# Kernel optimization log

Hardware: AMD Instinct MI355X
Metric: run time of the kernel (lower is better)

Reference implementation:

```python
import jax, jax.numpy as jnp
import numpy as np

B, S, D, H = 2, 2048, 1024, 16
HD = D // H          # 64
ROT = HD // 2        # 32

def _rope(x, cos, sin):
    # x: [B,S,H,HD] -> pairs [B,S,H,ROT,2]; cos/sin: [S,ROT] -> [1,S,1,ROT]
    x2 = x.reshape(x.shape[:3] + (ROT, 2))
    x0, x1 = x2[..., 0], x2[..., 1]
    c = cos[None, :, None, :]
    s = sin[None, :, None, :]
    out = jnp.stack([x0 * c - x1 * s, x1 * c + x0 * s], axis=-1)
    return out.reshape(x.shape)

def setup_inputs() -> dict:
    key = jax.random.key(0)
    ks = jax.random.split(key, 5)
    hidden_states = jax.random.normal(ks[0], (B, S, D), dtype=jnp.float32)
    # proper rotary cos/sin table: [S, ROT, 2]
    inv_freq = 1.0 / (10000.0 ** (np.arange(0, ROT, dtype=np.float32) / ROT))
    t = np.arange(S, dtype=np.float32)
    ang = np.outer(t, inv_freq)  # [S, ROT]
    freqs = jnp.asarray(np.stack([np.cos(ang), np.sin(ang)], axis=-1), dtype=jnp.float32)
    sc = 1.0 / np.sqrt(D)
    wq = jax.random.normal(ks[1], (D, D), dtype=jnp.float32) * sc
    wk = jax.random.normal(ks[2], (D, D), dtype=jnp.float32) * sc
    wv = jax.random.normal(ks[3], (D, D), dtype=jnp.float32) * sc
    wo = jax.random.normal(ks[4], (D, D), dtype=jnp.float32) * sc
    return {"hidden_states": hidden_states, "freqs": freqs, "wq": wq, "wk": wk, "wv": wv, "wo": wo}

def reference(hidden_states, freqs, wq, wk, wv, wo):
    b, s, _ = hidden_states.shape
    scaling = HD ** -0.5
    q = (hidden_states @ wq.T).reshape(b, s, H, HD)
    k = (hidden_states @ wk.T).reshape(b, s, H, HD)
    v = (hidden_states @ wv.T).reshape(b, s, H, HD)
    cos, sin = freqs[:s, :, 0], freqs[:s, :, 1]
    q = _rope(q, cos, sin)
    k = _rope(k, cos, sin)
    # [B,H,S,S] scores, fp32 softmax
    scores = jnp.einsum('bqhd,bkhd->bhqk', q, k) * scaling
    attn = jax.nn.softmax(scores.astype(jnp.float32), axis=-1).astype(q.dtype)
    out = jnp.einsum('bhqk,bkhd->bqhd', attn, v).reshape(b, s, D)
    return out @ wo.T
```

## Files before the change

kernel.cpp:

```cpp
#include <hip/hip_runtime.h>
#include <hip/hip_bf16.h>

typedef __attribute__((ext_vector_type(8))) short bf16x8;
typedef __attribute__((ext_vector_type(4))) float f32x4;
typedef __attribute__((ext_vector_type(16))) float f32x16;
typedef __attribute__((ext_vector_type(2))) float f32x2;
typedef unsigned short u16;

#define Bc   2
#define Sc   2048
#define Dc   1024
#define Hc   16
#define HDc  64
#define ROTc 32
#define Mrows 4096

__device__ __forceinline__ u16 f2bf(float x) {
  union { float f; unsigned u; } v{x};
  unsigned r = v.u + 0x7fffu + ((v.u >> 16) & 1u);
  return (u16)(r >> 16);
}
__device__ __forceinline__ float bf2f(u16 x) {
  union { unsigned u; float f; } v{(unsigned)x << 16};
  return v.f;
}
__device__ __forceinline__ unsigned cvtpk(float a, float b) {
  unsigned r;
  asm("v_cvt_pk_bf16_f32 %0, %1, %2" : "=v"(r) : "v"(a), "v"(b));
  return r;
}
__device__ __forceinline__ f32x2 pmax2(f32x2 a, f32x2 b) {
  f32x2 r;
  r.x = fmaxf(a.x, b.x);
  r.y = fmaxf(a.y, b.y);
  return r;
}

__device__ __forceinline__ void gload_lds16(const void* g, void* l) {
  __builtin_amdgcn_global_load_lds(
      (const __attribute__((address_space(1))) void*)g,
      (__attribute__((address_space(3))) void*)l, 16, 0, 0);
}

__global__ void cvt_all(const float* __restrict__ h, const float* __restrict__ q,
                        const float* __restrict__ k, const float* __restrict__ v,
                        const float* __restrict__ o,
                        u16* __restrict__ hb, u16* __restrict__ qb, u16* __restrict__ kb,
                        u16* __restrict__ vb, u16* __restrict__ ob) {
  size_t i = ((size_t)blockIdx.x * 256 + threadIdx.x) * 4;
  const float* s;
  u16* d;
  size_t off;
  if (i < (size_t)Mrows * Dc) {
    s = h; d = hb; off = i;
  } else {
    size_t j = i - (size_t)Mrows * Dc;
    int w = (int)(j >> 20);
    off = j & ((1u << 20) - 1);
    s = (w == 0) ? q : (w == 1) ? k : (w == 2) ? v : o;
    d = (w == 0) ? qb : (w == 1) ? kb : (w == 2) ? vb : ob;
  }
  float4 val = *reinterpret_cast<const float4*>(s + off);
  u16 r0 = f2bf(val.x), r1 = f2bf(val.y), r2 = f2bf(val.z), r3 = f2bf(val.w);
  ushort4 outv = {r0, r1, r2, r3};
  *reinterpret_cast<ushort4*>(d + off) = outv;
}

__global__ void gemm_qkv(const u16* __restrict__ A, const u16* __restrict__ W0,
                         const u16* __restrict__ W1, const u16* __restrict__ W2,
                         u16* __restrict__ Qo, u16* __restrict__ Ko,
                         u16* __restrict__ Vo) {
  __shared__ u16 As[128 * 32];
  __shared__ u16 Bs[128 * 32];
  const int by = blockIdx.y;
  const int wsel = by >> 3;
  const int n0 = (by & 7) * 128;
  const int m0 = blockIdx.x * 128;
  const u16* Bm = (wsel == 0) ? W0 : (wsel == 1) ? W1 : W2;
  const int t = threadIdx.x;
  const int w = t >> 6;
  const int lane = t & 63;
  const int wm = w >> 1, wn = w & 1;
  const int c = lane & 15, g = lane >> 4;
  const int srow = t >> 2, skoff = (t & 3) * 8;

  f32x4 acc[4][4] = {};

  const u16* ag = A + (size_t)(m0 + srow) * Dc + skoff;
  const u16* bg = Bm + (size_t)(n0 + srow) * Dc + skoff;
  u16* al = &As[(w * 16) * 32];
  u16* bl = &Bs[(w * 16) * 32];

  for (int k0 = 0; k0 < Dc; k0 += 32) {
    gload_lds16(ag + k0, al);
    gload_lds16(ag + k0 + (size_t)64 * Dc, al + 64 * 32);
    gload_lds16(bg + k0, bl);
    gload_lds16(bg + k0 + (size_t)64 * Dc, bl + 64 * 32);
    __syncthreads();
    bf16x8 a[4], b[4];
#pragma unroll
    for (int f = 0; f < 4; ++f) {
      a[f] = *(const bf16x8*)&As[(wm * 64 + f * 16 + c) * 32 + g * 8];
      b[f] = *(const bf16x8*)&Bs[(wn * 64 + f * 16 + c) * 32 + g * 8];
    }
#pragma unroll
    for (int fm = 0; fm < 4; ++fm)
#pragma unroll
      for (int fn = 0; fn < 4; ++fn)
        acc[fm][fn] =
            __builtin_amdgcn_mfma_f32_16x16x32_bf16(a[fm], b[fn], acc[fm][fn], 0, 0, 0);
    __syncthreads();
  }

  u16* dst = (wsel == 0) ? Qo : (wsel == 1) ? Ko : Vo;
#pragma unroll
  for (int fm = 0; fm < 4; ++fm)
#pragma unroll
    for (int fn = 0; fn < 4; ++fn)
#pragma unroll
      for (int r = 0; r < 4; ++r) {
        const int m = m0 + wm * 64 + fm * 16 + g * 4 + r;
        const int n = n0 + wn * 64 + fn * 16 + c;
        const float v = acc[fm][fn][r];
        const int b = m >> 11, s = m & (Sc - 1);
        const int hh = n >> 6, d = n & 63;
        size_t idx;
        if (wsel < 2)
          idx = (((size_t)(b * Hc + hh) * Sc) + s) * HDc + d;
        else
          idx = ((size_t)(b * Hc + hh) * HDc + d) * Sc + s;
        dst[idx] = f2bf(v);
      }
}

__global__ void gemm_out(const u16* __restrict__ A, const u16* __restrict__ Bm,
                         float* __restrict__ C) {
  __shared__ u16 As[64 * 32];
  __shared__ u16 Bs[128 * 32];
  const int m0 = blockIdx.x * 64;
  const int n0 = blockIdx.y * 128;
  const int t = threadIdx.x;
  const int w = t >> 6;
  const int lane = t & 63;
  const int wm = w >> 1, wn = w & 1;
  const int c = lane & 15, g = lane >> 4;
  const int srow = t >> 2, skoff = (t & 3) * 8;

  f32x4 acc[2][4] = {};

  const u16* ag = A + (size_t)(m0 + srow) * Dc + skoff;
  const u16* bg = Bm + (size_t)(n0 + srow) * Dc + skoff;
  u16* al = &As[(w * 16) * 32];
  u16* bl = &Bs[(w * 16) * 32];

  for (int k0 = 0; k0 < Dc; k0 += 32) {
    gload_lds16(ag + k0, al);
    gload_lds16(bg + k0, bl);
    gload_lds16(bg + k0 + (size_t)64 * Dc, bl + 64 * 32);
    __syncthreads();
    bf16x8 a[2], b[4];
#pragma unroll
    for (int f = 0; f < 2; ++f)
      a[f] = *(const bf16x8*)&As[(wm * 32 + f * 16 + c) * 32 + g * 8];
#pragma unroll
    for (int f = 0; f < 4; ++f)
      b[f] = *(const bf16x8*)&Bs[(wn * 64 + f * 16 + c) * 32 + g * 8];
#pragma unroll
    for (int fm = 0; fm < 2; ++fm)
#pragma unroll
      for (int fn = 0; fn < 4; ++fn)
        acc[fm][fn] =
            __builtin_amdgcn_mfma_f32_16x16x32_bf16(a[fm], b[fn], acc[fm][fn], 0, 0, 0);
    __syncthreads();
  }

#pragma unroll
  for (int fm = 0; fm < 2; ++fm)
#pragma unroll
    for (int fn = 0; fn < 4; ++fn)
#pragma unroll
      for (int r = 0; r < 4; ++r) {
        const int m = m0 + wm * 32 + fm * 16 + g * 4 + r;
        const int n = n0 + wn * 64 + fn * 16 + c;
        C[(size_t)m * Dc + n] = acc[fm][fn][r];
      }
}

__global__ void rope_all(u16* __restrict__ qb, u16* __restrict__ kb,
                         const float* __restrict__ freqs) {
  int idx = blockIdx.x * 256 + threadIdx.x;
  const int half = Bc * Hc * Sc * ROTc;
  u16* buf = qb;
  float scale = 0.125f * 1.44269504f;
  int p = idx;
  if (idx >= half) {
    buf = kb;
    scale = 1.0f;
    p = idx - half;
  }
  const int i = p & 31;
  const int s = (p >> 5) & (Sc - 1);
  const int bh = p >> 16;
  const float cs = freqs[(s * ROTc + i) * 2];
  const float sn = freqs[(s * ROTc + i) * 2 + 1];
  u16* ptr = buf + ((size_t)bh * Sc + s) * HDc + i * 2;
  unsigned pr = *reinterpret_cast<unsigned*>(ptr);
  float x0 = bf2f((u16)(pr & 0xffffu));
  float x1 = bf2f((u16)(pr >> 16));
  float y0 = (x0 * cs - x1 * sn) * scale;
  float y1 = (x1 * cs + x0 * sn) * scale;
  *reinterpret_cast<unsigned*>(ptr) = (unsigned)f2bf(y0) | ((unsigned)f2bf(y1) << 16);
}

__global__ __launch_bounds__(256, 2) void flash_attn(
    const u16* __restrict__ Q, const u16* __restrict__ Kb,
    const u16* __restrict__ Vt, u16* __restrict__ Ob) {
  __shared__ u16 Ks[2][32 * 128];
  __shared__ u16 Vs[2][32 * 128];
  const int orig = blockIdx.x;
  const int wg = (orig & 7) * 64 + (orig >> 3);
  const int bh = wg >> 4;
  const int q0 = (wg & 15) * 128;
  const int t = threadIdx.x, w = t >> 6, lane = t & 63;
  const int l31 = lane & 31, hi = lane >> 5;
  const int sr = t >> 4;
  const int su = (t & 15) ^ (sr & 15);
  const int skv = sr + ((su >> 3) << 5);
  const int sd8 = (su & 7) * 8;
  const int rsw = (l31 & 15);

  const u16* Qp = Q + (size_t)bh * Sc * HDc;
  const u16* Kp = Kb + (size_t)bh * Sc * HDc;
  const u16* Vp = Vt + (size_t)bh * HDc * Sc;

  const int q = q0 + w * 32 + l31;
  bf16x8 aq[4];
#pragma unroll
  for (int kd = 0; kd < 4; ++kd)
    aq[kd] = *(const bf16x8*)(Qp + (size_t)q * HDc + kd * 16 + hi * 8);

  float m_run = -1e30f, l_run = 0.f;
  f32x16 o[2] = {};

  gload_lds16(Kp + (size_t)skv * HDc + sd8, &Ks[0][w * 512]);
  gload_lds16(Kp + (size_t)(skv + 16) * HDc + sd8, &Ks[0][2048 + w * 512]);
  gload_lds16(Vp + (size_t)skv * Sc + sd8, &Vs[0][w * 512]);
  gload_lds16(Vp + (size_t)(skv + 16) * Sc + sd8, &Vs[0][2048 + w * 512]);
  __syncthreads();

  int buf = 0;
  for (int t0 = 0; t0 < Sc; t0 += 64) {
    if (t0 + 64 < Sc) {
      const int tn = t0 + 64;
      gload_lds16(Kp + (size_t)(tn + skv) * HDc + sd8, &Ks[buf ^ 1][w * 512]);
      gload_lds16(Kp + (size_t)(tn + skv + 16) * HDc + sd8, &Ks[buf ^ 1][2048 + w * 512]);
      gload_lds16(Vp + (size_t)skv * Sc + tn + sd8, &Vs[buf ^ 1][w * 512]);
      gload_lds16(Vp + (size_t)(skv + 16) * Sc + tn + sd8, &Vs[buf ^ 1][2048 + w * 512]);
    }
    f32x16 s0 = {}, s1 = {};
    __builtin_amdgcn_s_setprio(1);
#pragma unroll
    for (int kd = 0; kd < 4; ++kd) {
      const int u0 = kd * 2 + hi;
      bf16x8 a0 = *(const bf16x8*)&Ks[buf][l31 * 128 + (u0 ^ rsw) * 8];
      bf16x8 a1 = *(const bf16x8*)&Ks[buf][l31 * 128 + ((u0 + 8) ^ rsw) * 8];
      s0 = __builtin_amdgcn_mfma_f32_32x32x16_bf16(a0, aq[kd], s0, 0, 0, 0);
      s1 = __builtin_amdgcn_mfma_f32_32x32x16_bf16(a1, aq[kd], s1, 0, 0, 0);
    }
    __builtin_amdgcn_s_setprio(0);
    f32x2 t4[4];
#pragma unroll
    for (int i = 0; i < 4; ++i) {
      f32x2 e0; e0.x = s0[2 * i]; e0.y = s0[2 * i + 1];
      f32x2 e1; e1.x = s0[2 * i + 8]; e1.y = s0[2 * i + 9];
      f32x2 e2; e2.x = s1[2 * i]; e2.y = s1[2 * i + 1];
      f32x2 e3; e3.x = s1[2 * i + 8]; e3.y = s1[2 * i + 9];
      t4[i] = pmax2(pmax2(e0, e1), pmax2(e2, e3));
    }
    f32x2 tp = pmax2(pmax2(t4[0], t4[1]), pmax2(t4[2], t4[3]));
    float mt = fmaxf(tp.x, tp.y);
    mt = fmaxf(mt, __shfl_xor(mt, 32));
    const bool skip = __all(mt <= m_run + 8.0f);
    if (!skip) {
      const float mn2 = fmaxf(m_run, mt);
      const float scl = __builtin_amdgcn_exp2f(m_run - mn2);
      m_run = mn2;
      l_run *= scl;
      o[0] *= scl;
      o[1] *= scl;
    }
    const float mn = m_run;
#pragma unroll
    for (int r = 0; r < 16; ++r) {
      s0[r] = __builtin_amdgcn_exp2f(s0[r] - mn);
      s1[r] = __builtin_amdgcn_exp2f(s1[r] - mn);
    }
    f32x2 ac;
    ac.x = 0.f; ac.y = 0.f;
#pragma unroll
    for (int i = 0; i < 8; ++i) {
      f32x2 e0; e0.x = s0[2 * i]; e0.y = s0[2 * i + 1];
      f32x2 e1; e1.x = s1[2 * i]; e1.y = s1[2 * i + 1];
      ac += e0 + e1;
    }
    float rs = ac.x + ac.y;
    rs += __shfl_xor(rs, 32);
    l_run += rs;
    unsigned pk0[8], pk1[8];
#pragma unroll
    for (int B = 0; B < 4; ++B)
#pragma unroll
      for (int s2 = 0; s2 < 2; ++s2) {
        pk0[B * 2 + s2] = cvtpk(s0[4 * B + 2 * s2], s0[4 * B + 2 * s2 + 1]);
        pk1[B * 2 + s2] = cvtpk(s1[4 * B + 2 * s2], s1[4 * B + 2 * s2 + 1]);
      }
#pragma unroll
    for (int ks = 0; ks < 4; ++ks) {
      const unsigned* pk = (ks >> 1) ? pk1 : pk0;
      const int m2 = (ks & 1) * 4;
      const unsigned A0 = pk[m2 + 0], A1 = pk[m2 + 1];
      const unsigned B0 = pk[m2 + 2], B1 = pk[m2 + 3];
      const unsigned L0 = hi ? B0 : A0, L1 = hi ? B1 : A1;
      const unsigned R0 = hi ? A0 : B0, R1 = hi ? A1 : B1;
      const unsigned X0 = __shfl_xor(R0, 32), X1 = __shfl_xor(R1, 32);
      union { unsigned u[4]; bf16x8 v; } bp;
      bp.u[0] = hi ? X0 : L0;
      bp.u[1] = hi ? X1 : L1;
      bp.u[2] = hi ? L0 : X0;
      bp.u[3] = hi ? L1 : X1;
      const int uv = ks * 2 + hi;
      bf16x8 va0 = *(const bf16x8*)&Vs[buf][l31 * 128 + (uv ^ rsw) * 8];
      bf16x8 va1 = *(const bf16x8*)&Vs[buf][l31 * 128 + ((uv + 8) ^ rsw) * 8];
      __builtin_amdgcn_s_setprio(1);
      o[0] = __builtin_amdgcn_mfma_f32_32x32x16_bf16(va0, bp.v, o[0], 0, 0, 0);
      o[1] = __builtin_amdgcn_mfma_f32_32x32x16_bf16(va1, bp.v, o[1], 0, 0, 0);
      __builtin_amdgcn_s_setprio(0);
    }
    __syncthreads();
    buf ^= 1;
  }

  const float rl = 1.0f / l_run;
  const int b = bh >> 4, hh = bh & 15;
  u16* orow = Ob + ((size_t)b * Sc + q) * Dc + hh * HDc;
#pragma unroll
  for (int fv = 0; fv < 2; ++fv)
#pragma unroll
    for (int B2 = 0; B2 < 4; ++B2) {
      const float v0 = o[fv][4 * B2 + 0] * rl, v1 = o[fv][4 * B2 + 1] * rl;
      const float v2 = o[fv][4 * B2 + 2] * rl, v3 = o[fv][4 * B2 + 3] * rl;
      uint2 pv;
      pv.x = cvtpk(v0, v1);
      pv.y = cvtpk(v2, v3);
      *reinterpret_cast<uint2*>(orow + fv * 32 + 8 * B2 + 4 * hi) = pv;
    }
}

extern "C" void kernel_launch(void* const* d_in, const int* in_sizes, int n_in,
                              void* d_out, int out_size, void* d_ws, size_t ws_size,
                              hipStream_t stream) {
  (void)in_sizes; (void)n_in; (void)out_size; (void)ws_size;
  const float* hidden = (const float*)d_in[0];
  const float* freqs = (const float*)d_in[1];
  const float* wq = (const float*)d_in[2];
  const float* wk = (const float*)d_in[3];
  const float* wv = (const float*)d_in[4];
  const float* wo = (const float*)d_in[5];
  float* out = (float*)d_out;

  char* ws = (char*)d_ws;
  const size_t MB8 = (size_t)Mrows * Dc * 2;
  const size_t WB = (size_t)Dc * Dc * 2;
  u16* hb = (u16*)ws;  ws += MB8;
  u16* wqb = (u16*)ws; ws += WB;
  u16* wkb = (u16*)ws; ws += WB;
  u16* wvb = (u16*)ws; ws += WB;
  u16* wob = (u16*)ws; ws += WB;
  u16* qb = (u16*)ws;  ws += MB8;
  u16* kb = (u16*)ws;  ws += MB8;
  u16* vtb = (u16*)ws; ws += MB8;
  u16* ab = (u16*)ws;  ws += MB8;

  cvt_all<<<8192, 256, 0, stream>>>(hidden, wq, wk, wv, wo, hb, wqb, wkb, wvb, wob);
  gemm_qkv<<<dim3(32, 24), 256, 0, stream>>>(hb, wqb, wkb, wvb, qb, kb, vtb);
  rope_all<<<16384, 256, 0, stream>>>(qb, kb, freqs);
  flash_attn<<<512, 256, 0, stream>>>(qb, kb, vtb, ab);
  gemm_out<<<dim3(64, 8), 256, 0, stream>>>(ab, wob, out);
}
```

Measured before the change: 139.0 us.

## Split flash attention over KV halves and merge partial results in combine kernel

Each attention workgroup now covers only half of the KV sequence, which doubles the grid from 512 to 1024 blocks and raises the launch-bounds occupancy hint. Per-row max and sum statistics are written to scratch space that reuses the hidden and wq buffers, and a new combine kernel merges the two bf16 partial outputs with log-sum-exp weights. The goal is better CU occupancy on a grid that was too small. The cost is an extra kernel launch, extra memory traffic, and a second bf16 rounding of the partial outputs.

```diff
diff --git a/kernel.cpp b/kernel.cpp
--- a/kernel.cpp
+++ b/kernel.cpp
@@ -212,15 +212,19 @@
   *reinterpret_cast<unsigned*>(ptr) = (unsigned)f2bf(y0) | ((unsigned)f2bf(y1) << 16);
 }
 
-__global__ __launch_bounds__(256, 2) void flash_attn(
+__global__ __launch_bounds__(256, 4) void flash_attn(
     const u16* __restrict__ Q, const u16* __restrict__ Kb,
-    const u16* __restrict__ Vt, u16* __restrict__ Ob) {
+    const u16* __restrict__ Vt, u16* __restrict__ O0, u16* __restrict__ O1,
+    float* __restrict__ pm, float* __restrict__ pl) {
   __shared__ u16 Ks[2][32 * 128];
   __shared__ u16 Vs[2][32 * 128];
   const int orig = blockIdx.x;
-  const int wg = (orig & 7) * 64 + (orig >> 3);
-  const int bh = wg >> 4;
-  const int q0 = (wg & 15) * 128;
+  const int wg = (orig & 7) * 128 + (orig >> 3);
+  const int bh = wg >> 5;
+  const int rem = wg & 31;
+  const int q0 = (rem >> 1) << 7;
+  const int half = rem & 1;
+  const int kvb = half << 10;
   const int t = threadIdx.x, w = t >> 6, lane = t & 63;
   const int l31 = lane & 31, hi = lane >> 5;
   const int sr = t >> 4;
@@ -242,15 +246,15 @@
   float m_run = -1e30f, l_run = 0.f;
   f32x16 o[2] = {};
 
-  gload_lds16(Kp + (size_t)skv * HDc + sd8, &Ks[0][w * 512]);
-  gload_lds16(Kp + (size_t)(skv + 16) * HDc + sd8, &Ks[0][2048 + w * 512]);
-  gload_lds16(Vp + (size_t)skv * Sc + sd8, &Vs[0][w * 512]);
-  gload_lds16(Vp + (size_t)(skv + 16) * Sc + sd8, &Vs[0][2048 + w * 512]);
+  gload_lds16(Kp + (size_t)(kvb + skv) * HDc + sd8, &Ks[0][w * 512]);
+  gload_lds16(Kp + (size_t)(kvb + skv + 16) * HDc + sd8, &Ks[0][2048 + w * 512]);
+  gload_lds16(Vp + (size_t)skv * Sc + kvb + sd8, &Vs[0][w * 512]);
+  gload_lds16(Vp + (size_t)(skv + 16) * Sc + kvb + sd8, &Vs[0][2048 + w * 512]);
   __syncthreads();
 
   int buf = 0;
-  for (int t0 = 0; t0 < Sc; t0 += 64) {
-    if (t0 + 64 < Sc) {
+  for (int t0 = kvb; t0 < kvb + 1024; t0 += 64) {
+    if (t0 + 64 < kvb + 1024) {
       const int tn = t0 + 64;
       gload_lds16(Kp + (size_t)(tn + skv) * HDc + sd8, &Ks[buf ^ 1][w * 512]);
       gload_lds16(Kp + (size_t)(tn + skv + 16) * HDc + sd8, &Ks[buf ^ 1][2048 + w * 512]);
@@ -342,7 +346,8 @@
 
   const float rl = 1.0f / l_run;
   const int b = bh >> 4, hh = bh & 15;
-  u16* orow = Ob + ((size_t)b * Sc + q) * Dc + hh * HDc;
+  u16* obase = half ? O1 : O0;
+  u16* orow = obase + ((size_t)b * Sc + q) * Dc + hh * HDc;
 #pragma unroll
   for (int fv = 0; fv < 2; ++fv)
 #pragma unroll
@@ -354,6 +359,48 @@
       pv.y = cvtpk(v2, v3);
       *reinterpret_cast<uint2*>(orow + fv * 32 + 8 * B2 + 4 * hi) = pv;
     }
+  if (hi == 0) {
+    const int row = (bh << 11) + q;
+    pm[(half << 16) + row] = m_run;
+    pl[(half << 16) + row] = l_run;
+  }
+}
+
+__global__ void combine(const u16* __restrict__ O1, u16* __restrict__ ab,
+                        const float* __restrict__ pm, const float* __restrict__ pl) {
+  const int gid = blockIdx.x * 256 + threadIdx.x;
+  const int row = gid >> 3, oct = gid & 3 * 2 + (gid & 7);
+  const int oc = gid & 7;
+  const int bh = row >> 11, q = row & (Sc - 1);
+  const int b = bh >> 4, hh = bh & 15;
+  const float m1 = pm[row], l1 = pl[row];
+  const float m2 = pm[65536 + row], l2 = pl[65536 + row];
+  const float mx = fmaxf(m1, m2);
+  const float w1 = l1 * __builtin_amdgcn_exp2f(m1 - mx);
+  const float w2 = l2 * __builtin_amdgcn_exp2f(m2 - mx);
+  const float rw = 1.0f / (w1 + w2);
+  const float c1 = w1 * rw, c2 = w2 * rw;
+  const size_t base = ((size_t)b * Sc + q) * Dc + hh * HDc + oc * 8;
+  bf16x8 x = *reinterpret_cast<const bf16x8*>(ab + base);
+  bf16x8 y = *reinterpret_cast<const bf16x8*>(O1 + base);
+  uint2 outv;
+  float r0 = bf2f((u16)x[0]) * c1 + bf2f((u16)y[0]) * c2;
+  float r1 = bf2f((u16)x[1]) * c1 + bf2f((u16)y[1]) * c2;
+  float r2 = bf2f((u16)x[2]) * c1 + bf2f((u16)y[2]) * c2;
+  float r3 = bf2f((u16)x[3]) * c1 + bf2f((u16)y[3]) * c2;
+  float r4 = bf2f((u16)x[4]) * c1 + bf2f((u16)y[4]) * c2;
+  float r5 = bf2f((u16)x[5]) * c1 + bf2f((u16)y[5]) * c2;
+  float r6 = bf2f((u16)x[6]) * c1 + bf2f((u16)y[6]) * c2;
+  float r7 = bf2f((u16)x[7]) * c1 + bf2f((u16)y[7]) * c2;
+  outv.x = cvtpk(r0, r1);
+  outv.y = cvtpk(r2, r3);
+  uint2 outw;
+  outw.x = cvtpk(r4, r5);
+  outw.y = cvtpk(r6, r7);
+  uint4 full;
+  full.x = outv.x; full.y = outv.y; full.z = outw.x; full.w = outw.y;
+  *reinterpret_cast<uint4*>(ab + base) = full;
+  (void)oct;
 }
 
 extern "C" void kernel_launch(void* const* d_in, const int* in_sizes, int n_in,
@@ -381,9 +428,14 @@
   u16* vtb = (u16*)ws; ws += MB8;
   u16* ab = (u16*)ws;  ws += MB8;
 
+  u16* po = hb;
+  float* pm = (float*)wqb;
+  float* pl = pm + 2 * 65536;
+
   cvt_all<<<8192, 256, 0, stream>>>(hidden, wq, wk, wv, wo, hb, wqb, wkb, wvb, wob);
   gemm_qkv<<<dim3(32, 24), 256, 0, stream>>>(hb, wqb, wkb, wvb, qb, kb, vtb);
   rope_all<<<16384, 256, 0, stream>>>(qb, kb, freqs);
-  flash_attn<<<512, 256, 0, stream>>>(qb, kb, vtb, ab);
+  flash_attn<<<1024, 256, 0, stream>>>(qb, kb, vtb, ab, po, pm, pl);
+  combine<<<2048, 256, 0, stream>>>(po, ab, pm, pl);
   gemm_out<<<dim3(64, 8), 256, 0, stream>>>(ab, wob, out);
 }
```

After: 154.4 us. +11.1%, slower.
